# Performance work log

Measured on AMD Instinct MI355X. Metric: run time of the kernel, lower is better.

## Reference

```python
import jax, jax.numpy as jnp
import numpy as np
from math import pi
from jax.scipy.linalg import expm

N_QUBITS = 9
DIM = 256
BATCH = 64
HID = (4 + DIM) // 2
D = 2 ** N_QUBITS
INTERACTION_WEIGHT = 866.0 / (3.0 ** 6)


def setup_inputs() -> dict:
    key = jax.random.key(0)
    k = jax.random.split(key, 6)
    x = jax.random.normal(k[0], (BATCH, DIM), dtype=jnp.float32)
    mask_batch = jax.random.uniform(k[1], (BATCH, N_QUBITS), dtype=jnp.float32)
    upper = (jax.random.uniform(k[2], (N_QUBITS, N_QUBITS)) < 0.4).astype(jnp.float32)
    upper = jnp.triu(upper, 1)
    adj = upper + upper.T  # symmetric 0/1, zero diagonal
    W1 = jax.random.normal(k[3], (DIM, HID), dtype=jnp.float32) / np.sqrt(DIM).astype(np.float32)
    b1 = jnp.zeros((HID,), jnp.float32)
    W2 = jax.random.normal(k[4], (HID, 4), dtype=jnp.float32) / np.sqrt(HID).astype(np.float32)
    b2 = jnp.zeros((4,), jnp.float32)
    return {"x": x, "mask_batch": mask_batch, "adj": adj, "W1": W1, "b1": b1, "W2": W2, "b2": b2}


def _forward(x, mask_batch, adj, W1, b1, W2, b2):
    c64 = jnp.complex64
    n = N_QUBITS
    b = x.shape[0]
    # varyer MLP -> [raw_omega, delta, raw_phi, raw_time]
    v = jax.nn.relu(x @ W1 + b1) @ W2 + b2
    omega = jax.nn.softplus(v[:, 0])
    delta = v[:, 1]
    phi = jnp.mod(v[:, 2], 2.0 * pi)
    t = jax.nn.softplus(v[:, 3])
    sx = jnp.array([[0, 1], [1, 0]], dtype=c64)
    sy = jnp.array([[0, -1j], [1j, 0]], dtype=c64)
    nop = jnp.array([[1, 0], [0, 0]], dtype=c64)  # (I + sigma_z)/2
    # single-qubit Hamiltonian, (b, 2, 2)
    h = ((omega / 2)[:, None, None].astype(c64)
         * (jnp.cos(phi)[:, None, None] * sx - jnp.sin(phi)[:, None, None] * sy)
         - delta[:, None, None].astype(c64) * nop)
    # H_single = sum_j mask[b,j] * (I_{2^j} (x) h[b] (x) I_{2^{n-1-j}})
    H = jnp.zeros((b, D, D), dtype=c64)
    for j in range(n):  # structural loop over qubits (n fixed, small)
        L, R = 2 ** j, 2 ** (n - 1 - j)
        Ej = jnp.einsum('pq,bxy,rs->bpxrqys',
                        jnp.eye(L, dtype=c64), h, jnp.eye(R, dtype=c64)).reshape(b, D, D)
        H = H + mask_batch[:, j, None, None].astype(c64) * Ej
    # Interaction term: n_i n_j operators are diagonal in the computational basis.
    # kron ordering puts qubit 0 most significant; n_op = diag(1, 0) -> occ = 1 - bit.
    s = jnp.arange(D)
    bit = (s[:, None] >> (n - 1 - jnp.arange(n))[None, :]) & 1  # (D, n)
    occ = (1 - bit).astype(jnp.float32)
    Wmat = INTERACTION_WEIGHT * adj[None] * mask_batch[:, :, None] * mask_batch[:, None, :]  # (b,n,n)
    diag = jnp.einsum('bij,si,sj->bs', Wmat, occ, occ)  # (b, D)
    idx = jnp.arange(D)
    H = H.at[:, idx, idx].add(diag.astype(c64))
    # time evolution: psi = expm(-i t H) |0...0>  (first column of the propagator)
    M = (-1j) * t[:, None, None].astype(c64) * H
    exp_h = jax.vmap(expm)(M)
    return exp_h[:, :, 0]


def reference(x, mask_batch, adj, W1, b1, W2, b2):
    return _forward(x, mask_batch, adj, W1, b1, W2, b2)
```

## Files before the change

### kernel.cpp

```cpp
#include <hip/hip_runtime.h>
#include <math.h>

#define NQ     9
#define NDIM   256
#define NHID   130
#define NST    512
#define NBATCH 64
#define MCAP   460

__device__ __forceinline__ float softplusf(float x) {
    return (x > 0.f) ? (x + log1pf(expf(-x))) : log1pf(expf(x));
}

template<int CTRL>
__device__ __forceinline__ float dpp_f(float v) {
    int i = __float_as_int(v);
    return __int_as_float(__builtin_amdgcn_update_dpp(i, i, CTRL, 0xF, 0xF, false));
}
__device__ __forceinline__ float swzx16(float v) {
    return __int_as_float(__builtin_amdgcn_ds_swizzle(__float_as_int(v), 0x401F));
}
__device__ __forceinline__ float bperm(int addr, float v) {
    return __int_as_float(__builtin_amdgcn_ds_bpermute(addr, __float_as_int(v)));
}

typedef unsigned uint2v __attribute__((ext_vector_type(2)));

__device__ __forceinline__ float lx16(float v, bool hi) {
#if __has_builtin(__builtin_amdgcn_permlane16_swap)
    uint2v r = __builtin_amdgcn_permlane16_swap(__float_as_uint(v), __float_as_uint(v), false, false);
    return __uint_as_float(hi ? r[0] : r[1]);
#else
    return swzx16(v);
#endif
}
__device__ __forceinline__ float lx32(float v, bool hi, int bpaddr) {
#if __has_builtin(__builtin_amdgcn_permlane32_swap)
    uint2v r = __builtin_amdgcn_permlane32_swap(__float_as_uint(v), __float_as_uint(v), false, false);
    return __uint_as_float(hi ? r[0] : r[1]);
#else
    return bperm(bpaddr, v);
#endif
}

#define MV(NR, CR)                                                            \
  do {                                                                        \
    _Pragma("unroll")                                                         \
    for (int r = 0; r < 8; ++r) {                                             \
      const float a = CR[r];                                                  \
      float yr = dg2[r] * a;                                                  \
      yr = fmaf(in2[0], CR[r^1], yr);                                         \
      yr = fmaf(in2[1], CR[r^2], yr);                                         \
      yr = fmaf(in2[2], CR[r^4], yr);                                         \
      yr = fmaf(cx2[0], dpp_f<0xB1>(a), yr);                                  \
      yr = fmaf(cx2[1], dpp_f<0x4E>(a), yr);                                  \
      const float a7 = dpp_f<0x141>(a);                                       \
      yr = fmaf(cx2[2], dpp_f<0x1B>(a7), yr);                                 \
      yr = fmaf(cx2[3], dpp_f<0x140>(a7), yr);                                \
      yr = fmaf(cx2[4], lx16(a, h16), yr);                                    \
      yr = fmaf(cx2[5], lx32(a, h32, bpaddr), yr);                            \
      NR[r] = yr - NR[r];                                                     \
    }                                                                         \
  } while (0)

#define COEF(P, K)                                                            \
  do { const float ck = 2.0f * jlf[K];                                        \
    switch ((K) & 3) {                                                        \
      case 0: _Pragma("unroll") for (int r=0;r<8;++r) accr[r] += ck*P[r]; break; \
      case 1: _Pragma("unroll") for (int r=0;r<8;++r) acci[r] -= ck*P[r]; break; \
      case 2: _Pragma("unroll") for (int r=0;r<8;++r) accr[r] -= ck*P[r]; break; \
      case 3: _Pragma("unroll") for (int r=0;r<8;++r) acci[r] += ck*P[r]; break; \
    }                                                                         \
  } while (0)

__global__ __launch_bounds__(256) void fused_kernel(
    const float* __restrict__ x,    const float* __restrict__ mask,
    const float* __restrict__ adj,  const float* __restrict__ W1,
    const float* __restrict__ b1,   const float* __restrict__ W2,
    const float* __restrict__ b2,   float* __restrict__ out)
{
    const int b    = blockIdx.x;
    const int tid  = threadIdx.x;
    const int w    = tid >> 6;
    const int lane = tid & 63;

    __shared__ __align__(16) float w1s[NDIM * NHID];
    __shared__ float xs[NDIM];
    __shared__ float hs[NHID + 2];
    __shared__ float vs[4];
    __shared__ float ms[NQ];
    __shared__ float adjs[81];
    __shared__ float Wm[81];
    __shared__ double Ssh;

    {
        const float4* W14 = (const float4*)W1;
        float4* d4 = (float4*)w1s;
        #pragma unroll 4
        for (int i = tid; i < (NDIM*NHID)/4; i += 256) d4[i] = W14[i];
        if (tid < NDIM/4) ((float4*)xs)[tid] = ((const float4*)(x + b*NDIM))[tid];
        if (tid >= 64 && tid < 64 + NQ) ms[tid - 64] = mask[b*NQ + (tid - 64)];
        if (tid >= 128 && tid < 128 + 81) adjs[tid - 128] = adj[tid - 128];
    }
    __syncthreads();

    if (tid < NHID) {
        float a0 = b1[tid], a1 = 0.f;
        #pragma unroll 8
        for (int i = 0; i < NDIM; i += 2) {
            a0 = fmaf(xs[i],     w1s[i*NHID + tid],       a0);
            a1 = fmaf(xs[i + 1], w1s[(i + 1)*NHID + tid], a1);
        }
        hs[tid] = fmaxf(a0 + a1, 0.f);
    }
    __syncthreads();

    {
        float p = hs[lane]      * W2[lane*4 + w]
                + hs[lane + 64] * W2[(lane + 64)*4 + w];
        if (lane < 2) p += hs[128 + lane] * W2[(128 + lane)*4 + w];
        #pragma unroll
        for (int off = 32; off; off >>= 1) p += __shfl_down(p, off);
        if (lane == 0) vs[w] = p + b2[w];
    }
    __syncthreads();

    if (w != 0) return;

    double* fd  = (double*)w1s;
    float*  jlf = w1s + 2*(MCAP + 8);

    for (int e = lane; e < 81; e += 64) {
        int i = e / 9, j = e % 9;
        Wm[e] = (866.0f/729.0f) * adjs[e] * ms[i] * ms[j];
    }

    const float omega = softplusf(vs[0]);
    const float delta = vs[1];
    const float phi   = vs[2];
    const float t     = softplusf(vs[3]);
    const float halfw = 0.5f * omega;

    float oL[6];
    #pragma unroll
    for (int i = 0; i < 6; ++i) oL[i] = ((lane >> (5 - i)) & 1) ? 0.f : 1.f;
    float t1 = 0.f, moL = 0.f;
    for (int i = 0; i < 6; ++i) {
        moL = fmaf(ms[i], oL[i], moL);
        float row = 0.f;
        for (int j = 0; j < 6; ++j) row = fmaf(Wm[i*9 + j], oL[j], row);
        t1 = fmaf(oL[i], row, t1);
    }
    float g[3];
    for (int p = 0; p < 3; ++p) {
        float gp = 0.f;
        for (int i = 0; i < 6; ++i) gp = fmaf(Wm[i*9 + 6 + p], oL[i], gp);
        g[p] = gp;
    }
    const float w67 = Wm[6*9 + 7], w68 = Wm[6*9 + 8], w78 = Wm[7*9 + 8];
    float Dd[8];
    #pragma unroll
    for (int r = 0; r < 8; ++r) {
        const float o0 = (r & 4) ? 0.f : 1.f;
        const float o1 = (r & 2) ? 0.f : 1.f;
        const float o2 = (r & 1) ? 0.f : 1.f;
        const float cross = g[0]*o0 + g[1]*o1 + g[2]*o2;
        const float rr    = w67*o0*o1 + w68*o0*o2 + w78*o1*o2;
        const float mo_r  = moL + ms[6]*o0 + ms[7]*o1 + ms[8]*o2;
        Dd[r] = t1 + 2.f*(cross + rr) - delta*mo_r;
    }

    float mx = Dd[0], mn = Dd[0];
    #pragma unroll
    for (int r = 1; r < 8; ++r) { mx = fmaxf(mx, Dd[r]); mn = fminf(mn, Dd[r]); }
    #pragma unroll
    for (int off = 1; off < 64; off <<= 1) {
        mx = fmaxf(mx, __shfl_xor(mx, off));
        mn = fminf(mn, __shfl_xor(mn, off));
    }
    float sm = 0.f;
    for (int j = 0; j < NQ; ++j) sm += ms[j];
    const float c0   = 0.5f * (mx + mn);
    const float rho  = (0.5f * (mx - mn) + halfw * sm) * 1.003f;
    const float rhoE = fmaxf(rho, 1e-20f);
    const float zc   = t * rho;

    int M;
    const bool tiny = (zc < 0.5f);
    if (tiny) M = 8;
    else {
        M = (int)ceilf(zc + 3.5f * cbrtf(zc + 4.f) + 4.f);
        if (M > MCAP) M = MCAP;
    }

    if (tiny) {
        if (lane <= 8) {
            const float zh = 0.5f * zc;
            const float q  = zh * zh;
            float fact = 1.f;
            for (int i = 2; i <= lane; ++i) fact *= (float)i;
            const float pw = (lane == 0) ? 1.f : powf(zh, (float)lane);
            jlf[lane] = (pw / fact) *
                (1.f - q/(float)(lane+1) + 0.5f*q*q/(float)((lane+1)*(lane+2)));
        }
    } else {
        if (lane == 0) {
            const double zz  = (double)zc;
            const double inv = 1.0 / zz;
            const int   M2   = M + 20 + M/10;
            double fkp1 = 0.0, fk = 1e-30;
            for (int k = M2; k >= 1; --k) {
                double fkm1 = 2.0 * (double)k * inv * fk - fkp1;
                fkp1 = fk; fk = fkm1;
                const int idx = k - 1;
                if (idx <= M) fd[idx] = fk;
            }
            double S = fd[0];
            for (int idx = 2; idx <= M; idx += 2) S += 2.0 * fd[idx];
            Ssh = S;
        }
        for (int k = lane; k <= M; k += 64) jlf[k] = (float)(fd[k] / Ssh);
    }

    const float two_rho = 2.0f / rhoE;
    float dg2[8];
    #pragma unroll
    for (int r = 0; r < 8; ++r) dg2[r] = (Dd[r] - c0) * two_rho;
    float cx2[6];
    #pragma unroll
    for (int q = 0; q < 6; ++q) cx2[q] = ms[5 - q] * halfw * two_rho;
    float in2[3];
    #pragma unroll
    for (int p = 0; p < 3; ++p) in2[p] = ms[8 - p] * halfw * two_rho;
    const int  bpaddr = (lane ^ 32) << 2;
    const bool h16    = (lane & 16) != 0;
    const bool h32    = (lane & 32) != 0;

    float p0[8], p1[8], accr[8], acci[8];
    #pragma unroll
    for (int r = 0; r < 8; ++r) { p0[r] = 0.f; p1[r] = 0.f; acci[r] = 0.f; }
    p0[0] = (lane == 0) ? 1.f : 0.f;

    const float J0 = jlf[0];
    #pragma unroll
    for (int r = 0; r < 8; ++r) accr[r] = J0 * p0[r];

    MV(p1, p0);
    #pragma unroll
    for (int r = 0; r < 8; ++r) p1[r] *= 0.5f;
    { const float c1 = 2.0f * jlf[1];
      #pragma unroll
      for (int r = 0; r < 8; ++r) acci[r] -= c1 * p1[r]; }

    int k = 2;
    while (k <= M) {
        MV(p0, p1);
        COEF(p0, k);
        ++k;
        if (k > M) break;
        MV(p1, p0);
        COEF(p1, k);
        ++k;
    }

    const float base = t * c0;
    const float pcl  = (float)__popc(lane);
    float o[8];
    #pragma unroll
    for (int r = 0; r < 8; ++r) {
        const float beta = base + phi * (pcl + (float)__popc(r));
        float sb, cbta;
        __sincosf(beta, &sb, &cbta);
        o[r] = accr[r]*cbta + acci[r]*sb;
    }
    float4* o4 = (float4*)(out + b*NST + (lane << 3));
    o4[0] = make_float4(o[0], o[1], o[2], o[3]);
    o4[1] = make_float4(o[4], o[5], o[6], o[7]);
}

extern "C" void kernel_launch(void* const* d_in, const int* in_sizes, int n_in,
                              void* d_out, int out_size, void* d_ws, size_t ws_size,
                              hipStream_t stream) {
    const float *x = nullptr, *msk = nullptr, *adj = nullptr,
                *W1 = nullptr, *b1 = nullptr, *W2 = nullptr, *b2 = nullptr;
    for (int i = 0; i < n_in; ++i) {
        const float* p = (const float*)d_in[i];
        switch (in_sizes[i]) {
            case 16384: x   = p; break;
            case 576:   msk = p; break;
            case 81:    adj = p; break;
            case 33280: W1  = p; break;
            case 130:   b1  = p; break;
            case 520:   W2  = p; break;
            case 4:     b2  = p; break;
            default: break;
        }
    }
    fused_kernel<<<NBATCH, 256, 0, stream>>>(x, msk, adj, W1, b1, W2, b2,
                                             (float*)d_out);
}
```

Baseline: 25.30 us.

## Use direct global-to-LDS loads, trim Chebyshev order, and restructure recurrence loop

Staging of W1 and x into shared memory now goes through the global_load_lds builtin, so the copy bypasses registers. The Chebyshev truncation order M is reduced with tighter constants, which cuts matrix-vector iterations but risks accuracy. The first recurrence step is computed analytically from the basis vector, and the main loop becomes a single non-unrolled body that swaps buffers each step. The output phases now use a rotation recurrence instead of eight sincos calls, and the tiny-z case replaces powf with repeated multiplication. The buffer swap and disabled unroll may add register moves per iteration.

New measurement: 26.72 us. 1.06x slower.

```diff
diff --git a/kernel.cpp b/kernel.cpp
--- a/kernel.cpp
+++ b/kernel.cpp
@@ -8,6 +8,8 @@
 #define NBATCH 64
 #define MCAP   460
 
+typedef unsigned uint2v __attribute__((ext_vector_type(2)));
+
 __device__ __forceinline__ float softplusf(float x) {
     return (x > 0.f) ? (x + log1pf(expf(-x))) : log1pf(expf(x));
 }
@@ -23,9 +25,6 @@
 __device__ __forceinline__ float bperm(int addr, float v) {
     return __int_as_float(__builtin_amdgcn_ds_bpermute(addr, __float_as_int(v)));
 }
-
-typedef unsigned uint2v __attribute__((ext_vector_type(2)));
-
 __device__ __forceinline__ float lx16(float v, bool hi) {
 #if __has_builtin(__builtin_amdgcn_permlane16_swap)
     uint2v r = __builtin_amdgcn_permlane16_swap(__float_as_uint(v), __float_as_uint(v), false, false);
@@ -40,6 +39,16 @@
     return __uint_as_float(hi ? r[0] : r[1]);
 #else
     return bperm(bpaddr, v);
+#endif
+}
+
+__device__ __forceinline__ void gl_lds16(const float4* g, float4* l) {
+#if __has_builtin(__builtin_amdgcn_global_load_lds)
+    __builtin_amdgcn_global_load_lds(
+        (const __attribute__((address_space(1))) void*)g,
+        (__attribute__((address_space(3))) void*)l, 16, 0, 0);
+#else
+    *l = *g;
 #endif
 }
 
@@ -63,16 +72,6 @@
     }                                                                         \
   } while (0)
 
-#define COEF(P, K)                                                            \
-  do { const float ck = 2.0f * jlf[K];                                        \
-    switch ((K) & 3) {                                                        \
-      case 0: _Pragma("unroll") for (int r=0;r<8;++r) accr[r] += ck*P[r]; break; \
-      case 1: _Pragma("unroll") for (int r=0;r<8;++r) acci[r] -= ck*P[r]; break; \
-      case 2: _Pragma("unroll") for (int r=0;r<8;++r) accr[r] -= ck*P[r]; break; \
-      case 3: _Pragma("unroll") for (int r=0;r<8;++r) acci[r] += ck*P[r]; break; \
-    }                                                                         \
-  } while (0)
-
 __global__ __launch_bounds__(256) void fused_kernel(
     const float* __restrict__ x,    const float* __restrict__ mask,
     const float* __restrict__ adj,  const float* __restrict__ W1,
@@ -85,7 +84,7 @@
     const int lane = tid & 63;
 
     __shared__ __align__(16) float w1s[NDIM * NHID];
-    __shared__ float xs[NDIM];
+    __shared__ __align__(16) float xs[NDIM];
     __shared__ float hs[NHID + 2];
     __shared__ float vs[4];
     __shared__ float ms[NQ];
@@ -96,9 +95,13 @@
     {
         const float4* W14 = (const float4*)W1;
         float4* d4 = (float4*)w1s;
-        #pragma unroll 4
-        for (int i = tid; i < (NDIM*NHID)/4; i += 256) d4[i] = W14[i];
-        if (tid < NDIM/4) ((float4*)xs)[tid] = ((const float4*)(x + b*NDIM))[tid];
+        const int wb = tid & ~63;
+        for (int it = 0; it < 32; ++it)
+            gl_lds16(W14 + it*256 + tid, d4 + it*256 + wb);
+        if (tid < 128)
+            gl_lds16(W14 + 8192 + tid, d4 + 8192 + wb);
+        if (tid < 64)
+            gl_lds16((const float4*)(x + b*NDIM) + tid, (float4*)xs);
         if (tid >= 64 && tid < 64 + NQ) ms[tid - 64] = mask[b*NQ + (tid - 64)];
         if (tid >= 128 && tid < 128 + 81) adjs[tid - 128] = adj[tid - 128];
     }
@@ -189,7 +192,7 @@
     const bool tiny = (zc < 0.5f);
     if (tiny) M = 8;
     else {
-        M = (int)ceilf(zc + 3.5f * cbrtf(zc + 4.f) + 4.f);
+        M = (int)ceilf(zc + 3.2f * cbrtf(zc + 4.f) + 3.5f);
         if (M > MCAP) M = MCAP;
     }
 
@@ -197,9 +200,9 @@
         if (lane <= 8) {
             const float zh = 0.5f * zc;
             const float q  = zh * zh;
-            float fact = 1.f;
+            float fact = 1.f, pw = 1.f;
             for (int i = 2; i <= lane; ++i) fact *= (float)i;
-            const float pw = (lane == 0) ? 1.f : powf(zh, (float)lane);
+            for (int i = 0; i < lane; ++i) pw *= zh;
             jlf[lane] = (pw / fact) *
                 (1.f - q/(float)(lane+1) + 0.5f*q*q/(float)((lane+1)*(lane+2)));
         }
@@ -236,42 +239,69 @@
     const bool h16    = (lane & 16) != 0;
     const bool h32    = (lane & 32) != 0;
 
-    float p0[8], p1[8], accr[8], acci[8];
-    #pragma unroll
-    for (int r = 0; r < 8; ++r) { p0[r] = 0.f; p1[r] = 0.f; acci[r] = 0.f; }
-    p0[0] = (lane == 0) ? 1.f : 0.f;
-
-    const float J0 = jlf[0];
-    #pragma unroll
-    for (int r = 0; r < 8; ++r) accr[r] = J0 * p0[r];
-
-    MV(p1, p0);
-    #pragma unroll
-    for (int r = 0; r < 8; ++r) p1[r] *= 0.5f;
+    float A[8], B[8], accr[8], acci[8];
+    #pragma unroll
+    for (int r = 0; r < 8; ++r) { A[r] = 0.f; B[r] = 0.f; acci[r] = 0.f; accr[r] = 0.f; }
+    A[0] = (lane == 0) ? 1.f : 0.f;
+    if (lane == 0) {
+        B[0] = 0.5f * dg2[0];
+        B[1] = 0.5f * in2[0];
+        B[2] = 0.5f * in2[1];
+        B[4] = 0.5f * in2[2];
+    } else if (lane == 1 || lane == 2 || lane == 4 || lane == 8 || lane == 16 || lane == 32) {
+        const int q = 31 - __clz(lane);
+        B[0] = 0.5f * cx2[q];
+    }
+    accr[0] = jlf[0] * A[0];
     { const float c1 = 2.0f * jlf[1];
       #pragma unroll
-      for (int r = 0; r < 8; ++r) acci[r] -= c1 * p1[r]; }
+      for (int r = 0; r < 8; ++r) acci[r] -= c1 * B[r]; }
 
     int k = 2;
+    #pragma clang loop unroll(disable)
     while (k <= M) {
-        MV(p0, p1);
-        COEF(p0, k);
+        MV(A, B);
+        { const float ck = 2.0f * jlf[k];
+          switch (k & 3) {
+            case 0: { _Pragma("unroll") for (int r=0;r<8;++r) accr[r] += ck*A[r]; } break;
+            case 1: { _Pragma("unroll") for (int r=0;r<8;++r) acci[r] -= ck*A[r]; } break;
+            case 2: { _Pragma("unroll") for (int r=0;r<8;++r) accr[r] -= ck*A[r]; } break;
+            case 3: { _Pragma("unroll") for (int r=0;r<8;++r) acci[r] += ck*A[r]; } break;
+          }
+        }
+        #pragma unroll
+        for (int r = 0; r < 8; ++r) { const float tp = A[r]; A[r] = B[r]; B[r] = tp; }
         ++k;
-        if (k > M) break;
-        MV(p1, p0);
-        COEF(p1, k);
-        ++k;
-    }
-
-    const float base = t * c0;
-    const float pcl  = (float)__popc(lane);
+    }
+
+    const float pcl = (float)__popc(lane);
+    float C[4], S[4];
+    {
+        float s0, c0b, su, cu;
+        __sincosf(t * c0 + phi * pcl, &s0, &c0b);
+        __sincosf(phi, &su, &cu);
+        C[0] = c0b; S[0] = s0;
+        #pragma clang loop unroll(disable)
+        for (int n = 1; n < 4; ++n) {
+            C[n] = C[n-1]*cu - S[n-1]*su;
+            S[n] = S[n-1]*cu + C[n-1]*su;
+        }
+    }
+    {
+        float c = C[0], s = S[0], su, cu;
+        __sincosf(phi, &su, &cu);
+        #pragma unroll
+        for (int n = 1; n < 4; ++n) {
+            const float cn = c*cu - s*su;
+            const float sn = s*cu + c*su;
+            C[n] = cn; S[n] = sn; c = cn; s = sn;
+        }
+    }
     float o[8];
     #pragma unroll
     for (int r = 0; r < 8; ++r) {
-        const float beta = base + phi * (pcl + (float)__popc(r));
-        float sb, cbta;
-        __sincosf(beta, &sb, &cbta);
-        o[r] = accr[r]*cbta + acci[r]*sb;
+        const int n = __popc(r);
+        o[r] = accr[r]*C[n] + acci[r]*S[n];
     }
     float4* o4 = (float4*)(out + b*NST + (lane << 3));
     o4[0] = make_float4(o[0], o[1], o[2], o[3]);
```
